# Kernel tuning notes

Hardware: AMD Instinct MI355X
Metric: run time of the kernel (lower is better)

The kernel has to match this reference:

```python
import jax, jax.numpy as jnp
import numpy as np

D_MODEL = 1024
N_HEADS = 16
HEAD_DIM = D_MODEL // N_HEADS
WINDOW = 256
N_GLOBAL = 2
EPS = 1e-5


def _layernorm(x, g, b):
    mu = jnp.mean(x, axis=-1, keepdims=True)
    var = jnp.var(x, axis=-1, keepdims=True)
    return (x - mu) * jax.lax.rsqrt(var + EPS) * g + b


def _longformer_mask(T):
    i = jnp.arange(T)[:, None]
    j = jnp.arange(T)[None, :]
    half = WINDOW // 2
    local = (j >= i - half) & (j <= i + half)
    glob = jnp.zeros((T, T), dtype=bool)
    if N_GLOBAL >= 1:
        glob = glob | (i == 0) | (j == 0)
    if N_GLOBAL >= 2 and T > 1:
        glob = glob | (i == T - 1) | (j == T - 1)
    allowed = (local | glob) & (j <= i)  # causal
    neg_inf = jnp.float32(-jnp.inf)
    return jnp.where(allowed, jnp.float32(0.0), neg_inf)[None, None]  # (1,1,T,T)


def setup_inputs() -> dict:
    key = jax.random.key(0)
    ks = jax.random.split(key, 8)
    B, T, D = 2, 2048, D_MODEL
    s = 0.02
    return {
        "x": jax.random.normal(ks[0], (B, T, D), dtype=jnp.float32),
        "ln1_g": jnp.ones((D,), jnp.float32),
        "ln1_b": jnp.zeros((D,), jnp.float32),
        "ln2_g": jnp.ones((D,), jnp.float32),
        "ln2_b": jnp.zeros((D,), jnp.float32),
        "Wq": jax.random.normal(ks[1], (D, D), jnp.float32) * s,
        "Wk": jax.random.normal(ks[2], (D, D), jnp.float32) * s,
        "Wv": jax.random.normal(ks[3], (D, D), jnp.float32) * s,
        "Wo": jax.random.normal(ks[4], (D, D), jnp.float32) * s,
        "bo": jnp.zeros((D,), jnp.float32),
        "W1": jax.random.normal(ks[5], (D, 4 * D), jnp.float32) * s,
        "b1": jnp.zeros((4 * D,), jnp.float32),
        "W2": jax.random.normal(ks[6], (4 * D, D), jnp.float32) * s,
        "b2": jnp.zeros((D,), jnp.float32),
    }


def reference(x, ln1_g, ln1_b, ln2_g, ln2_b, Wq, Wk, Wv, Wo, bo, W1, b1, W2, b2):
    B, T, D = x.shape
    h = _layernorm(x, ln1_g, ln1_b)
    # (B,T,D) -> (B,H,T,hd)
    q = (h @ Wq).reshape(B, T, N_HEADS, HEAD_DIM).transpose(0, 2, 1, 3)
    k = (h @ Wk).reshape(B, T, N_HEADS, HEAD_DIM).transpose(0, 2, 1, 3)
    v = (h @ Wv).reshape(B, T, N_HEADS, HEAD_DIM).transpose(0, 2, 1, 3)
    mask = _longformer_mask(T)
    scores = jnp.einsum("bhqd,bhkd->bhqk", q, k) / np.sqrt(HEAD_DIM) + mask
    attn = jax.nn.softmax(scores, axis=-1)
    out = jnp.einsum("bhqk,bhkd->bhqd", attn, v)
    out = out.transpose(0, 2, 1, 3).reshape(B, T, D)
    x = x + out @ Wo + bo
    h2 = _layernorm(x, ln2_g, ln2_b)
    ffn = jax.nn.gelu(h2 @ W1 + b1, approximate=False) @ W2 + b2
    return x + ffn
```

## Files before the change

### kernel.cpp

```cpp
#include <hip/hip_runtime.h>
#include <cmath>

#define Tseq 2048
#define Dm   1024
#define NHd  16
#define HDim 64
#define Mrows 4096
#define QS   3072
#define PAD  72
#define NSPLIT 16

typedef _Float16 f16;
typedef _Float16 half8 __attribute__((ext_vector_type(8)));
typedef _Float16 half4 __attribute__((ext_vector_type(4)));
typedef float    floatx4 __attribute__((ext_vector_type(4)));

#define ASYNC_COPY16(g, l)                                                       \
  __builtin_amdgcn_global_load_lds((const __attribute__((address_space(1))) void*)(g), \
                                   (__attribute__((address_space(3))) void*)(l), 16, 0, 0)

__device__ __forceinline__ float gelu_f(float v) {
  const float u = 0.7978845608028654f * (v + 0.044715f * v * v * v);
  const float e = __expf(2.0f * u);
  return 0.5f * v * (2.0f - 2.0f / (e + 1.0f));
}

__device__ __forceinline__ void transp_body(const float* __restrict__ W,
                                            f16* __restrict__ Wt, int K, int N,
                                            int bx, int by, float (*tile)[33]) {
  const int n0 = bx * 32, k0 = by * 32;
  const int tx = threadIdx.x & 31, ty = threadIdx.x >> 5;
#pragma unroll
  for (int i = 0; i < 32; i += 8)
    tile[ty + i][tx] = W[(size_t)(k0 + ty + i) * N + n0 + tx];
  __syncthreads();
#pragma unroll
  for (int i = 0; i < 32; i += 8)
    Wt[(size_t)(n0 + ty + i) * K + k0 + tx] = (f16)tile[tx][ty + i];
}

__global__ __launch_bounds__(256) void prep(const float* __restrict__ Wq,
                                            const float* __restrict__ Wk,
                                            const float* __restrict__ Wv,
                                            const float* __restrict__ Wo,
                                            const float* __restrict__ W1,
                                            const float* __restrict__ W2,
                                            const float* __restrict__ x,
                                            const float* __restrict__ g,
                                            const float* __restrict__ bb,
                                            f16* __restrict__ WqkvT,
                                            f16* __restrict__ WoT,
                                            f16* __restrict__ W1T,
                                            f16* __restrict__ W2T,
                                            f16* __restrict__ hF) {
  __shared__ float tile[32][33];
  __shared__ float red[8];
  const int lin = blockIdx.x;
  if (lin < 4096) {
    const int wsel = lin >> 10, t = lin & 1023;
    const float* W = (wsel == 0) ? Wq : (wsel == 1) ? Wk : (wsel == 2) ? Wv : Wo;
    f16* dst = (wsel < 3) ? (WqkvT + (size_t)wsel * Dm * Dm) : WoT;
    transp_body(W, dst, Dm, Dm, t & 31, t >> 5, tile);
    return;
  }
  if (lin < 8192) {
    const int t = lin - 4096;
    transp_body(W1, W1T, Dm, 4 * Dm, t & 127, t >> 7, tile);
    return;
  }
  if (lin < 12288) {
    const int t = lin - 8192;
    transp_body(W2, W2T, 4 * Dm, Dm, t & 31, t >> 5, tile);
    return;
  }
  const int row = lin - 12288, t = threadIdx.x;
  const float4 v = ((const float4*)(x + (size_t)row * Dm))[t];
  float s  = v.x + v.y + v.z + v.w;
  float ss = v.x * v.x + v.y * v.y + v.z * v.z + v.w * v.w;
#pragma unroll
  for (int m = 32; m >= 1; m >>= 1) { s += __shfl_xor(s, m); ss += __shfl_xor(ss, m); }
  if ((t & 63) == 0) { red[t >> 6] = s; red[4 + (t >> 6)] = ss; }
  __syncthreads();
  const float S  = red[0] + red[1] + red[2] + red[3];
  const float SS = red[4] + red[5] + red[6] + red[7];
  const float mean = S * (1.0f / Dm);
  const float inv  = rsqrtf(SS * (1.0f / Dm) - mean * mean + 1e-5f);
  const float4 gg = ((const float4*)g)[t];
  const float4 bv = ((const float4*)bb)[t];
  half4 o;
  o.x = (f16)(((v.x - mean) * inv) * gg.x + bv.x);
  o.y = (f16)(((v.y - mean) * inv) * gg.y + bv.y);
  o.z = (f16)(((v.z - mean) * inv) * gg.z + bv.z);
  o.w = (f16)(((v.w - mean) * inv) * gg.w + bv.w);
  *((half4*)(hF + (size_t)row * Dm) + t) = o;
}

template <int NS>
__global__ __launch_bounds__(256) void reduce_ln(const f16* __restrict__ P,
                                                 const float* __restrict__ resid,
                                                 const float* __restrict__ bias,
                                                 const float* __restrict__ g,
                                                 const float* __restrict__ bb,
                                                 float* __restrict__ x1,
                                                 f16* __restrict__ h) {
  const int row = blockIdx.x, t = threadIdx.x;
  const size_t idx = (size_t)row * (Dm / 4) + t;
  const float4 r = ((const float4*)resid)[idx];
  const float4 b = ((const float4*)bias)[t];
  float4 o; o.x = r.x + b.x; o.y = r.y + b.y; o.z = r.z + b.z; o.w = r.w + b.w;
#pragma unroll
  for (int z = 0; z < NS; ++z) {
    const half4 p = ((const half4*)(P + (size_t)z * Mrows * Dm))[idx];
    o.x += (float)p[0]; o.y += (float)p[1]; o.z += (float)p[2]; o.w += (float)p[3];
  }
  ((float4*)x1)[idx] = o;
  float s  = o.x + o.y + o.z + o.w;
  float ss = o.x * o.x + o.y * o.y + o.z * o.z + o.w * o.w;
#pragma unroll
  for (int m = 32; m >= 1; m >>= 1) { s += __shfl_xor(s, m); ss += __shfl_xor(ss, m); }
  __shared__ float red[8];
  if ((t & 63) == 0) { red[t >> 6] = s; red[4 + (t >> 6)] = ss; }
  __syncthreads();
  const float S  = red[0] + red[1] + red[2] + red[3];
  const float SS = red[4] + red[5] + red[6] + red[7];
  const float mean = S * (1.0f / Dm);
  const float inv  = rsqrtf(SS * (1.0f / Dm) - mean * mean + 1e-5f);
  const float4 gg = ((const float4*)g)[t];
  const float4 bv = ((const float4*)bb)[t];
  half4 oh;
  oh[0] = (f16)(((o.x - mean) * inv) * gg.x + bv.x);
  oh[1] = (f16)(((o.y - mean) * inv) * gg.y + bv.y);
  oh[2] = (f16)(((o.z - mean) * inv) * gg.z + bv.z);
  oh[3] = (f16)(((o.w - mean) * inv) * gg.w + bv.w);
  ((half4*)h)[idx] = oh;
}

template <int NS>
__global__ __launch_bounds__(256) void reduceK(const f16* __restrict__ P,
                                               const float* __restrict__ resid,
                                               const float* __restrict__ bias,
                                               float* __restrict__ out) {
  const int t = blockIdx.x * 256 + threadIdx.x;
  const int col4 = t & (Dm / 4 - 1);
  const float4 r = ((const float4*)resid)[t];
  const float4 b = ((const float4*)bias)[col4];
  float4 o; o.x = r.x + b.x; o.y = r.y + b.y; o.z = r.z + b.z; o.w = r.w + b.w;
#pragma unroll
  for (int z = 0; z < NS; ++z) {
    const half4 p = ((const half4*)(P + (size_t)z * Mrows * Dm))[t];
    o.x += (float)p[0]; o.y += (float)p[1]; o.z += (float)p[2]; o.w += (float)p[3];
  }
  ((float4*)out)[t] = o;
}

template <int EPI, int LNZ>
__global__ __launch_bounds__(256, 4) void gemm_f16(const f16* __restrict__ A,
                                                   const f16* __restrict__ Bt,
                                                   int M, int N, int K, int kLen,
                                                   const float* __restrict__ bias,
                                                   f16* __restrict__ Ch) {
  constexpr int NZ = 1 << LNZ;
  __shared__ f16 As[128 * 64];
  __shared__ f16 Bs[128 * 64];
  const int tid = threadIdx.x;
  int bx, by, bz;
  if (EPI == 5) {
    const int lin = blockIdx.x;
    bz = lin & (NZ - 1);
    bx = (lin >> LNZ) & 7;
    by = lin >> (LNZ + 3);
  } else {
    const int nbx = N >> 7, chunk = nbx >> 3;
    const int xcd = blockIdx.x & 7, idx = blockIdx.x >> 3;
    bx = xcd * chunk + idx % chunk;
    by = idx / chunk;
    bz = 0;
  }
  const int m0 = by * 128, n0 = bx * 128;
  const int kOff = bz * kLen;
  const int w = tid >> 6, l = tid & 63;
  const int wr = (w >> 1) * 64, wc = (w & 1) * 64;
  const int c = l & 15, qq = l >> 4;
  const int cx = c & 7;
  const int srow = tid >> 3;
  const int scol = ((tid & 7) ^ (srow & 7)) * 8;

  floatx4 acc[4][4] = {};

  const f16* Ab = A + (size_t)(m0 + srow) * K + kOff + scol;
  const f16* Bb = Bt + (size_t)(n0 + srow) * K + kOff + scol;

  for (int k0 = 0; k0 < kLen; k0 += 64) {
    __syncthreads();
#pragma unroll
    for (int i = 0; i < 4; ++i) {
      ASYNC_COPY16(Ab + k0 + (size_t)(i * 32) * K, As + i * 2048 + w * 512);
      ASYNC_COPY16(Bb + k0 + (size_t)(i * 32) * K, Bs + i * 2048 + w * 512);
    }
    __syncthreads();
    half8 af[4][2], bfr[4][2];
#pragma unroll
    for (int t = 0; t < 4; ++t) {
      const int ra = (wr + t * 16 + c) * 64;
      af[t][0] = *(const half8*)&As[ra + ((qq ^ cx) * 8)];
      af[t][1] = *(const half8*)&As[ra + (((4 + qq) ^ cx) * 8)];
      const int rb = (wc + t * 16 + c) * 64;
      bfr[t][0] = *(const half8*)&Bs[rb + ((qq ^ cx) * 8)];
      bfr[t][1] = *(const half8*)&Bs[rb + (((4 + qq) ^ cx) * 8)];
    }
#pragma unroll
    for (int ti = 0; ti < 4; ++ti)
#pragma unroll
      for (int tj = 0; tj < 4; ++tj) {
        acc[ti][tj] = __builtin_amdgcn_mfma_f32_16x16x32_f16(af[ti][0], bfr[tj][0], acc[ti][tj], 0, 0, 0);
        acc[ti][tj] = __builtin_amdgcn_mfma_f32_16x16x32_f16(af[ti][1], bfr[tj][1], acc[ti][tj], 0, 0, 0);
      }
  }

  f16* Cw = (EPI == 5) ? (Ch + (size_t)bz * M * N) : Ch;
#pragma unroll
  for (int ti = 0; ti < 4; ++ti)
#pragma unroll
    for (int tj = 0; tj < 4; ++tj)
#pragma unroll
      for (int r = 0; r < 4; ++r) {
        const int row = m0 + wr + ti * 16 + qq * 4 + r;
        const int col = n0 + wc + tj * 16 + c;
        const size_t idx = (size_t)row * N + col;
        float v = acc[ti][tj][r];
        if (EPI == 2) {
          Cw[idx] = (f16)gelu_f(v + bias[col]);
        } else {
          Cw[idx] = (f16)v;
        }
      }
}

__global__ __launch_bounds__(256, 4) void attn_fused(const f16* __restrict__ qkv,
                                                     f16* __restrict__ ao,
                                                     float* __restrict__ part) {
  __shared__ f16 qs[64 * PAD];
  __shared__ f16 ks[64 * PAD];
  __shared__ f16 vts[64 * PAD];
  __shared__ f16 ps[64 * PAD];
  const int lin = blockIdx.x;
  const int tid = threadIdx.x;

  if (lin >= 1024) {
    const int r_ = lin - 1024;
    const int bh = r_ & 31, sp = r_ >> 5;
    const int b = bh >> 4, hh = bh & 15;
    const size_t base = ((size_t)b * Tseq) * QS + hh * HDim;
    const int j0 = sp * (Tseq / NSPLIT);
    float* qsh  = (float*)qs;
    float* psf  = (float*)ks;
    float* red  = (float*)vts;
    float* red2 = red + 4;
    float (*oaccp)[64] = (float(*)[64])ps;
    if (tid < 64) qsh[tid] = (float)qkv[base + (size_t)(Tseq - 1) * QS + tid] * 0.125f;
    __syncthreads();
    float sv = -INFINITY;
    if (tid < 128) {
      const f16* kr = qkv + base + 1024 + (size_t)(j0 + tid) * QS;
      float a0 = 0.f;
#pragma unroll
      for (int d8 = 0; d8 < 8; ++d8) {
        const half8 kv = *(const half8*)(kr + d8 * 8);
#pragma unroll
        for (int e = 0; e < 8; ++e) a0 = fmaf((float)kv[e], qsh[d8 * 8 + e], a0);
      }
      sv = a0;
    }
    float mx = sv;
#pragma unroll
    for (int mm = 32; mm >= 1; mm >>= 1) mx = fmaxf(mx, __shfl_xor(mx, mm));
    if ((tid & 63) == 0) red[tid >> 6] = mx;
    __syncthreads();
    const float M = fmaxf(red[0], red[1]);
    float p = 0.f;
    if (tid < 128) { p = __expf(sv - M); psf[tid] = p; }
    float sum = p;
#pragma unroll
    for (int mm = 32; mm >= 1; mm >>= 1) sum += __shfl_xor(sum, mm);
    if ((tid & 63) == 0) red2[tid >> 6] = sum;
    __syncthreads();
    const float L = red2[0] + red2[1];
    const int d = tid & 63, pt = tid >> 6;
    const f16* vb = qkv + base + 2048 + d;
    float acc = 0.f;
    for (int j = pt * 32; j < pt * 32 + 32; ++j)
      acc = fmaf(psf[j], (float)vb[(size_t)(j0 + j) * QS], acc);
    oaccp[pt][d] = acc;
    __syncthreads();
    if (tid < 64) {
      const float o = oaccp[0][tid] + oaccp[1][tid] + oaccp[2][tid] + oaccp[3][tid];
      float* dst = part + ((size_t)bh * NSPLIT + sp) * 66;
      dst[tid] = o;
      if (tid == 0) { dst[64] = M; dst[65] = L; }
    }
    return;
  }

  const int qt = lin & 31;
  const int byv = lin >> 5;
  const int b = byv >> 4, hh = byv & 15;
  const int q0 = qt * 64;
  const int w = tid >> 6, l = tid & 63;
  const int c = l & 15, qq = l >> 4;
  const int wr = w * 16;
  const size_t base = ((size_t)b * Tseq) * QS + hh * HDim;
  const int rr = tid >> 2, ss = (tid & 3) * 16;

  {
    const f16* src = qkv + base + (size_t)(q0 + rr) * QS + ss;
    *(uint4*)&qs[rr * PAD + ss]     = *(const uint4*)src;
    *(uint4*)&qs[rr * PAD + ss + 8] = *(const uint4*)(src + 8);
  }

  float m_run[4], l_run[4];
  floatx4 oacc[4];
#pragma unroll
  for (int r = 0; r < 4; ++r) { m_run[r] = -INFINITY; l_run[r] = 0.f; }
#pragma unroll
  for (int td = 0; td < 4; ++td) oacc[td] = (floatx4){0.f, 0.f, 0.f, 0.f};

  int chunks[4]; int nch = 0;
  if (qt > 2) chunks[nch++] = 0;
  for (int ch = (qt - 2 > 0 ? qt - 2 : 0); ch <= qt; ++ch) chunks[nch++] = ch;

  for (int ci = 0; ci < nch; ++ci) {
    const int j0 = chunks[ci] * 64;
    __syncthreads();
    {
      const f16* srck = qkv + base + 1024 + (size_t)(j0 + rr) * QS + ss;
      *(uint4*)&ks[rr * PAD + ss]     = *(const uint4*)srck;
      *(uint4*)&ks[rr * PAD + ss + 8] = *(const uint4*)(srck + 8);
      const f16* srcv = qkv + base + 2048 + (size_t)(j0 + rr) * QS + ss;
      uint4 va0 = *(const uint4*)srcv;
      uint4 va1 = *(const uint4*)(srcv + 8);
      const f16* e0 = (const f16*)&va0;
      const f16* e1 = (const f16*)&va1;
#pragma unroll
      for (int i = 0; i < 8; ++i) vts[(ss + i) * PAD + rr] = e0[i];
#pragma unroll
      for (int i = 0; i < 8; ++i) vts[(ss + 8 + i) * PAD + rr] = e1[i];
    }
    __syncthreads();

    const half8 a0 = *(const half8*)&qs[(wr + c) * PAD + qq * 8];
    const half8 a1 = *(const half8*)&qs[(wr + c) * PAD + 32 + qq * 8];
    floatx4 sacc[4];
#pragma unroll
    for (int tj = 0; tj < 4; ++tj) {
      const half8 b0 = *(const half8*)&ks[(tj * 16 + c) * PAD + qq * 8];
      const half8 b1 = *(const half8*)&ks[(tj * 16 + c) * PAD + 32 + qq * 8];
      floatx4 s4 = {0.f, 0.f, 0.f, 0.f};
      s4 = __builtin_amdgcn_mfma_f32_16x16x32_f16(a0, b0, s4, 0, 0, 0);
      s4 = __builtin_amdgcn_mfma_f32_16x16x32_f16(a1, b1, s4, 0, 0, 0);
      sacc[tj] = s4;
    }

#pragma unroll
    for (int r = 0; r < 4; ++r) {
      const int ii = q0 + wr + qq * 4 + r;
      float sv[4];
      float mx = -INFINITY;
#pragma unroll
      for (int tj = 0; tj < 4; ++tj) {
        const int jj = j0 + tj * 16 + c;
        const bool allowed = (jj <= ii) && ((ii - jj) <= 128 || jj == 0);
        sv[tj] = allowed ? sacc[tj][r] * 0.125f : -INFINITY;
        mx = fmaxf(mx, sv[tj]);
      }
#pragma unroll
      for (int mm = 8; mm >= 1; mm >>= 1) mx = fmaxf(mx, __shfl_xor(mx, mm));
      const float mn = fmaxf(m_run[r], mx);
      const float alpha = (mn == -INFINITY) ? 1.f : __expf(m_run[r] - mn);
      float sum = 0.f;
      float p[4];
#pragma unroll
      for (int tj = 0; tj < 4; ++tj) { p[tj] = __expf(sv[tj] - mn); sum += p[tj]; }
#pragma unroll
      for (int mm = 8; mm >= 1; mm >>= 1) sum += __shfl_xor(sum, mm);
      l_run[r] = l_run[r] * alpha + sum;
      m_run[r] = mn;
#pragma unroll
      for (int td = 0; td < 4; ++td) oacc[td][r] *= alpha;
#pragma unroll
      for (int tj = 0; tj < 4; ++tj)
        ps[(wr + qq * 4 + r) * PAD + tj * 16 + c] = (f16)p[tj];
    }

    const half8 p0 = *(const half8*)&ps[(wr + c) * PAD + qq * 8];
    const half8 p1 = *(const half8*)&ps[(wr + c) * PAD + 32 + qq * 8];
#pragma unroll
    for (int td = 0; td < 4; ++td) {
      const half8 b0 = *(const half8*)&vts[(td * 16 + c) * PAD + qq * 8];
      const half8 b1 = *(const half8*)&vts[(td * 16 + c) * PAD + 32 + qq * 8];
      oacc[td] = __builtin_amdgcn_mfma_f32_16x16x32_f16(p0, b0, oacc[td], 0, 0, 0);
      oacc[td] = __builtin_amdgcn_mfma_f32_16x16x32_f16(p1, b1, oacc[td], 0, 0, 0);
    }
  }

#pragma unroll
  for (int td = 0; td < 4; ++td)
#pragma unroll
    for (int r = 0; r < 4; ++r) {
      const int ii = q0 + wr + qq * 4 + r;
      ao[((size_t)(b * Tseq + ii)) * Dm + hh * HDim + td * 16 + c] =
          (f16)(oacc[td][r] / l_run[r]);
    }
}

__global__ __launch_bounds__(64) void attn_row_comb(const float* __restrict__ part,
                                                    f16* __restrict__ ao) {
  const int bh = blockIdx.x;
  const int b = bh >> 4, hh = bh & 15;
  const int tid = threadIdx.x;
  const float* pp = part + (size_t)bh * NSPLIT * 66;
  float M = -INFINITY;
#pragma unroll
  for (int s = 0; s < NSPLIT; ++s) M = fmaxf(M, pp[s * 66 + 64]);
  float L = 0.f, o = 0.f;
#pragma unroll
  for (int s = 0; s < NSPLIT; ++s) {
    const float wgt = __expf(pp[s * 66 + 64] - M);
    L += pp[s * 66 + 65] * wgt;
    o += pp[s * 66 + tid] * wgt;
  }
  ao[((size_t)(b * Tseq + Tseq - 1)) * Dm + hh * HDim + tid] = (f16)(o / L);
}

extern "C" void kernel_launch(void* const* d_in, const int* in_sizes, int n_in,
                              void* d_out, int out_size, void* d_ws, size_t ws_size,
                              hipStream_t stream) {
  (void)in_sizes; (void)n_in; (void)out_size; (void)ws_size;
  const float* x    = (const float*)d_in[0];
  const float* ln1g = (const float*)d_in[1];
  const float* ln1b = (const float*)d_in[2];
  const float* ln2g = (const float*)d_in[3];
  const float* ln2b = (const float*)d_in[4];
  const float* Wq   = (const float*)d_in[5];
  const float* Wk   = (const float*)d_in[6];
  const float* Wv   = (const float*)d_in[7];
  const float* Wo   = (const float*)d_in[8];
  const float* bo   = (const float*)d_in[9];
  const float* W1   = (const float*)d_in[10];
  const float* b1   = (const float*)d_in[11];
  const float* W2   = (const float*)d_in[12];
  const float* b2   = (const float*)d_in[13];
  float* out = (float*)d_out;

  char* w0 = (char*)d_ws;
  size_t off = 0;
  auto take = [&](size_t bytes) -> char* {
    char* p = w0 + off;
    off += (bytes + 255) & ~(size_t)255;
    return p;
  };
  f16*   WqkvT = (f16*)take((size_t)3 * Dm * Dm * 2);
  f16*   WoT   = (f16*)take((size_t)Dm * Dm * 2);
  f16*   W1T   = (f16*)take((size_t)Dm * 4 * Dm * 2);
  f16*   W2T   = (f16*)take((size_t)Dm * 4 * Dm * 2);
  f16*   hF    = (f16*)take((size_t)Mrows * Dm * 2);
  f16*   qkvh  = (f16*)take((size_t)Mrows * QS * 2);
  f16*   attnF = (f16*)take((size_t)Mrows * Dm * 2);
  float* x1    = (float*)take((size_t)Mrows * Dm * 4);
  f16*   h2F   = (f16*)take((size_t)Mrows * Dm * 2);
  f16*   pbuf  = (f16*)take((size_t)4 * Mrows * Dm * 2);
  float* rowp  = (float*)take((size_t)32 * NSPLIT * 66 * 4);
  f16*   ffn1F = qkvh;

  const dim3 blk(256);

  prep<<<dim3(16384), blk, 0, stream>>>(Wq, Wk, Wv, Wo, W1, W2, x, ln1g, ln1b,
                                        WqkvT, WoT, W1T, W2T, hF);

  gemm_f16<3, 0><<<dim3(768), blk, 0, stream>>>(
      hF, WqkvT, Mrows, QS, Dm, Dm, nullptr, qkvh);

  attn_fused<<<dim3(1536), blk, 0, stream>>>(qkvh, attnF, rowp);
  attn_row_comb<<<dim3(2 * NHd), dim3(64), 0, stream>>>(rowp, attnF);

  gemm_f16<5, 1><<<dim3(512), blk, 0, stream>>>(
      attnF, WoT, Mrows, Dm, Dm, Dm / 2, nullptr, pbuf);
  reduce_ln<2><<<Mrows, blk, 0, stream>>>(pbuf, x, bo, ln2g, ln2b, x1, h2F);

  gemm_f16<2, 0><<<dim3(1024), blk, 0, stream>>>(
      h2F, W1T, Mrows, 4 * Dm, Dm, Dm, b1, ffn1F);

  gemm_f16<5, 2><<<dim3(1024), blk, 0, stream>>>(
      ffn1F, W2T, Mrows, Dm, 4 * Dm, Dm, nullptr, pbuf);
  reduceK<4><<<Mrows * Dm / 1024, blk, 0, stream>>>(pbuf, x1, b2, out);
}
```

Measured before the change: 314.9 us.

## Merge global-row attention into one block per head, prefetch K/V, widen reduceK

```diff
diff --git a/kernel.cpp b/kernel.cpp
--- a/kernel.cpp
+++ b/kernel.cpp
@@ -8,7 +8,6 @@
 #define Mrows 4096
 #define QS   3072
 #define PAD  72
-#define NSPLIT 16
 
 typedef _Float16 f16;
 typedef _Float16 half8 __attribute__((ext_vector_type(8)));
@@ -141,16 +140,22 @@
                                                const float* __restrict__ bias,
                                                float* __restrict__ out) {
   const int t = blockIdx.x * 256 + threadIdx.x;
-  const int col4 = t & (Dm / 4 - 1);
-  const float4 r = ((const float4*)resid)[t];
-  const float4 b = ((const float4*)bias)[col4];
-  float4 o; o.x = r.x + b.x; o.y = r.y + b.y; o.z = r.z + b.z; o.w = r.w + b.w;
+  const int col8 = t & (Dm / 8 - 1);
+  const float4 r0 = ((const float4*)resid)[2 * t];
+  const float4 r1 = ((const float4*)resid)[2 * t + 1];
+  const float4 b0 = ((const float4*)bias)[2 * col8];
+  const float4 b1 = ((const float4*)bias)[2 * col8 + 1];
+  float4 o0, o1;
+  o0.x = r0.x + b0.x; o0.y = r0.y + b0.y; o0.z = r0.z + b0.z; o0.w = r0.w + b0.w;
+  o1.x = r1.x + b1.x; o1.y = r1.y + b1.y; o1.z = r1.z + b1.z; o1.w = r1.w + b1.w;
 #pragma unroll
   for (int z = 0; z < NS; ++z) {
-    const half4 p = ((const half4*)(P + (size_t)z * Mrows * Dm))[t];
-    o.x += (float)p[0]; o.y += (float)p[1]; o.z += (float)p[2]; o.w += (float)p[3];
-  }
-  ((float4*)out)[t] = o;
+    const half8 p = ((const half8*)(P + (size_t)z * Mrows * Dm))[t];
+    o0.x += (float)p[0]; o0.y += (float)p[1]; o0.z += (float)p[2]; o0.w += (float)p[3];
+    o1.x += (float)p[4]; o1.y += (float)p[5]; o1.z += (float)p[6]; o1.w += (float)p[7];
+  }
+  ((float4*)out)[2 * t]     = o0;
+  ((float4*)out)[2 * t + 1] = o1;
 }
 
 template <int EPI, int LNZ>
@@ -237,8 +242,7 @@
 }
 
 __global__ __launch_bounds__(256, 4) void attn_fused(const f16* __restrict__ qkv,
-                                                     f16* __restrict__ ao,
-                                                     float* __restrict__ part) {
+                                                     f16* __restrict__ ao) {
   __shared__ f16 qs[64 * PAD];
   __shared__ f16 ks[64 * PAD];
   __shared__ f16 vts[64 * PAD];
@@ -247,21 +251,22 @@
   const int tid = threadIdx.x;
 
   if (lin >= 1024) {
-    const int r_ = lin - 1024;
-    const int bh = r_ & 31, sp = r_ >> 5;
+    const int bh = lin - 1024;
     const int b = bh >> 4, hh = bh & 15;
     const size_t base = ((size_t)b * Tseq) * QS + hh * HDim;
-    const int j0 = sp * (Tseq / NSPLIT);
     float* qsh  = (float*)qs;
-    float* psf  = (float*)ks;
+    float* psf  = (float*)ps;
     float* red  = (float*)vts;
     float* red2 = red + 4;
-    float (*oaccp)[64] = (float(*)[64])ps;
+    float (*oaccp)[64] = (float(*)[64])ks;
     if (tid < 64) qsh[tid] = (float)qkv[base + (size_t)(Tseq - 1) * QS + tid] * 0.125f;
     __syncthreads();
-    float sv = -INFINITY;
-    if (tid < 128) {
-      const f16* kr = qkv + base + 1024 + (size_t)(j0 + tid) * QS;
+    float sv[8];
+    float mx = -INFINITY;
+#pragma unroll
+    for (int jj = 0; jj < 8; ++jj) {
+      const int j = jj * 256 + tid;
+      const f16* kr = qkv + base + 1024 + (size_t)j * QS;
       float a0 = 0.f;
 #pragma unroll
       for (int d8 = 0; d8 < 8; ++d8) {
@@ -269,34 +274,38 @@
 #pragma unroll
         for (int e = 0; e < 8; ++e) a0 = fmaf((float)kv[e], qsh[d8 * 8 + e], a0);
       }
-      sv = a0;
-    }
-    float mx = sv;
+      sv[jj] = a0;
+      mx = fmaxf(mx, a0);
+    }
 #pragma unroll
     for (int mm = 32; mm >= 1; mm >>= 1) mx = fmaxf(mx, __shfl_xor(mx, mm));
     if ((tid & 63) == 0) red[tid >> 6] = mx;
     __syncthreads();
-    const float M = fmaxf(red[0], red[1]);
-    float p = 0.f;
-    if (tid < 128) { p = __expf(sv - M); psf[tid] = p; }
-    float sum = p;
+    const float M = fmaxf(fmaxf(red[0], red[1]), fmaxf(red[2], red[3]));
+    float sum = 0.f;
+#pragma unroll
+    for (int jj = 0; jj < 8; ++jj) {
+      const float p = __expf(sv[jj] - M);
+      psf[jj * 256 + tid] = p;
+      sum += p;
+    }
 #pragma unroll
     for (int mm = 32; mm >= 1; mm >>= 1) sum += __shfl_xor(sum, mm);
     if ((tid & 63) == 0) red2[tid >> 6] = sum;
     __syncthreads();
-    const float L = red2[0] + red2[1];
+    const float L = red2[0] + red2[1] + red2[2] + red2[3];
     const int d = tid & 63, pt = tid >> 6;
-    const f16* vb = qkv + base + 2048 + d;
+    const f16* vr = qkv + base + 2048 + d + (size_t)(pt * 512) * QS;
+    const float* pp = psf + pt * 512;
     float acc = 0.f;
-    for (int j = pt * 32; j < pt * 32 + 32; ++j)
-      acc = fmaf(psf[j], (float)vb[(size_t)(j0 + j) * QS], acc);
+#pragma unroll 4
+    for (int j = 0; j < 512; ++j)
+      acc = fmaf(pp[j], (float)vr[(size_t)j * QS], acc);
     oaccp[pt][d] = acc;
     __syncthreads();
     if (tid < 64) {
       const float o = oaccp[0][tid] + oaccp[1][tid] + oaccp[2][tid] + oaccp[3][tid];
-      float* dst = part + ((size_t)bh * NSPLIT + sp) * 66;
-      dst[tid] = o;
-      if (tid == 0) { dst[64] = M; dst[65] = L; }
+      ao[((size_t)(b * Tseq + Tseq - 1)) * Dm + hh * HDim + tid] = (f16)(o / L);
     }
     return;
   }
@@ -328,24 +337,40 @@
   if (qt > 2) chunks[nch++] = 0;
   for (int ch = (qt - 2 > 0 ? qt - 2 : 0); ch <= qt; ++ch) chunks[nch++] = ch;
 
+  uint4 kr0, kr1, vr0, vr1;
+  {
+    const int j0 = chunks[0] * 64;
+    const f16* srck = qkv + base + 1024 + (size_t)(j0 + rr) * QS + ss;
+    kr0 = *(const uint4*)srck;
+    kr1 = *(const uint4*)(srck + 8);
+    const f16* srcv = qkv + base + 2048 + (size_t)(j0 + rr) * QS + ss;
+    vr0 = *(const uint4*)srcv;
+    vr1 = *(const uint4*)(srcv + 8);
+  }
+
   for (int ci = 0; ci < nch; ++ci) {
     const int j0 = chunks[ci] * 64;
     __syncthreads();
     {
-      const f16* srck = qkv + base + 1024 + (size_t)(j0 + rr) * QS + ss;
-      *(uint4*)&ks[rr * PAD + ss]     = *(const uint4*)srck;
-      *(uint4*)&ks[rr * PAD + ss + 8] = *(const uint4*)(srck + 8);
-      const f16* srcv = qkv + base + 2048 + (size_t)(j0 + rr) * QS + ss;
-      uint4 va0 = *(const uint4*)srcv;
-      uint4 va1 = *(const uint4*)(srcv + 8);
-      const f16* e0 = (const f16*)&va0;
-      const f16* e1 = (const f16*)&va1;
+      *(uint4*)&ks[rr * PAD + ss]     = kr0;
+      *(uint4*)&ks[rr * PAD + ss + 8] = kr1;
+      const f16* e0 = (const f16*)&vr0;
+      const f16* e1 = (const f16*)&vr1;
 #pragma unroll
       for (int i = 0; i < 8; ++i) vts[(ss + i) * PAD + rr] = e0[i];
 #pragma unroll
       for (int i = 0; i < 8; ++i) vts[(ss + 8 + i) * PAD + rr] = e1[i];
     }
     __syncthreads();
+    if (ci + 1 < nch) {
+      const int j1 = chunks[ci + 1] * 64;
+      const f16* srck = qkv + base + 1024 + (size_t)(j1 + rr) * QS + ss;
+      kr0 = *(const uint4*)srck;
+      kr1 = *(const uint4*)(srck + 8);
+      const f16* srcv = qkv + base + 2048 + (size_t)(j1 + rr) * QS + ss;
+      vr0 = *(const uint4*)srcv;
+      vr1 = *(const uint4*)(srcv + 8);
+    }
 
     const half8 a0 = *(const half8*)&qs[(wr + c) * PAD + qq * 8];
     const half8 a1 = *(const half8*)&qs[(wr + c) * PAD + 32 + qq * 8];
@@ -407,28 +432,10 @@
 #pragma unroll
     for (int r = 0; r < 4; ++r) {
       const int ii = q0 + wr + qq * 4 + r;
-      ao[((size_t)(b * Tseq + ii)) * Dm + hh * HDim + td * 16 + c] =
-          (f16)(oacc[td][r] / l_run[r]);
-    }
-}
-
-__global__ __launch_bounds__(64) void attn_row_comb(const float* __restrict__ part,
-                                                    f16* __restrict__ ao) {
-  const int bh = blockIdx.x;
-  const int b = bh >> 4, hh = bh & 15;
-  const int tid = threadIdx.x;
-  const float* pp = part + (size_t)bh * NSPLIT * 66;
-  float M = -INFINITY;
-#pragma unroll
-  for (int s = 0; s < NSPLIT; ++s) M = fmaxf(M, pp[s * 66 + 64]);
-  float L = 0.f, o = 0.f;
-#pragma unroll
-  for (int s = 0; s < NSPLIT; ++s) {
-    const float wgt = __expf(pp[s * 66 + 64] - M);
-    L += pp[s * 66 + 65] * wgt;
-    o += pp[s * 66 + tid] * wgt;
-  }
-  ao[((size_t)(b * Tseq + Tseq - 1)) * Dm + hh * HDim + tid] = (f16)(o / L);
+      if (ii != Tseq - 1)
+        ao[((size_t)(b * Tseq + ii)) * Dm + hh * HDim + td * 16 + c] =
+            (f16)(oacc[td][r] / l_run[r]);
+    }
 }
 
 extern "C" void kernel_launch(void* const* d_in, const int* in_sizes, int n_in,
@@ -468,7 +475,6 @@
   float* x1    = (float*)take((size_t)Mrows * Dm * 4);
   f16*   h2F   = (f16*)take((size_t)Mrows * Dm * 2);
   f16*   pbuf  = (f16*)take((size_t)4 * Mrows * Dm * 2);
-  float* rowp  = (float*)take((size_t)32 * NSPLIT * 66 * 4);
   f16*   ffn1F = qkvh;
 
   const dim3 blk(256);
@@ -479,8 +485,7 @@
   gemm_f16<3, 0><<<dim3(768), blk, 0, stream>>>(
       hF, WqkvT, Mrows, QS, Dm, Dm, nullptr, qkvh);
 
-  attn_fused<<<dim3(1536), blk, 0, stream>>>(qkvh, attnF, rowp);
-  attn_row_comb<<<dim3(2 * NHd), dim3(64), 0, stream>>>(rowp, attnF);
+  attn_fused<<<dim3(1056), blk, 0, stream>>>(qkvh, attnF);
 
   gemm_f16<5, 1><<<dim3(512), blk, 0, stream>>>(
       attnF, WoT, Mrows, Dm, Dm, Dm / 2, nullptr, pbuf);
@@ -491,5 +496,5 @@
 
   gemm_f16<5, 2><<<dim3(1024), blk, 0, stream>>>(
       ffn1F, W2T, Mrows, Dm, 4 * Dm, Dm, nullptr, pbuf);
-  reduceK<4><<<Mrows * Dm / 1024, blk, 0, stream>>>(pbuf, x1, b2, out);
-}
+  reduceK<4><<<Mrows * Dm / (256 * 8), blk, 0, stream>>>(pbuf, x1, b2, out);
+}
```

Result: slower. 375.1 us (+19.1%).
